# Optimization experiments

Measured on AMD Instinct MI355X. Metric: run time of the kernel, lower is better.

## Reference

```python
import jax, jax.numpy as jnp
import numpy as np

N = 100000
E = 1600000
IN_C = 64
HID = 128
EPS = 1e-5


def _glorot(key, shape):
    fan_in, fan_out = shape[1], shape[0]
    lim = float(np.sqrt(6.0 / (fan_in + fan_out)))
    return jax.random.uniform(key, shape, jnp.float32, -lim, lim)


def setup_inputs() -> dict:
    key = jax.random.key(0)
    ks = jax.random.split(key, 12)
    x = jax.random.normal(ks[0], (N, IN_C), jnp.float32)
    edge_index = jax.random.randint(ks[1], (2, E), 0, N, jnp.int64)
    return {
        "x": x,
        "edge_index": edge_index,
        # SAGEConv layer 0: lin_l (neighbor, with bias), lin_r (root, no bias)
        "Wl0": _glorot(ks[2], (HID, IN_C)), "bl0": jnp.zeros((HID,), jnp.float32),
        "Wr0": _glorot(ks[3], (HID, IN_C)),
        "g0": jnp.ones((HID,), jnp.float32), "be0": jnp.zeros((HID,), jnp.float32),
        # SAGEConv layer 1
        "Wl1": _glorot(ks[4], (HID, HID)), "bl1": jnp.zeros((HID,), jnp.float32),
        "Wr1": _glorot(ks[5], (HID, HID)),
        "g1": jnp.ones((HID,), jnp.float32), "be1": jnp.zeros((HID,), jnp.float32),
        # MLP head: hidden -> hidden//2 -> 1
        "W1": _glorot(ks[6], (HID // 2, HID)), "b1": jnp.zeros((HID // 2,), jnp.float32),
        "W2": _glorot(ks[7], (1, HID // 2)), "b2": jnp.zeros((1,), jnp.float32),
    }


def _sage_max(x, src, dst, Wl, bl, Wr):
    # gather source features along edges, scatter-max into destination nodes
    msgs = x[src]                                             # [E, d]
    agg = jax.ops.segment_max(msgs, dst, num_segments=N)      # [N, d], -inf if empty
    agg = jnp.where(jnp.isfinite(agg), agg, 0.0)              # empty neighborhoods -> 0 (PyG scatter)
    return agg @ Wl.T + bl + x @ Wr.T


def _layernorm(x, g, b):
    mu = jnp.mean(x, axis=-1, keepdims=True)
    var = jnp.var(x, axis=-1, keepdims=True)
    return (x - mu) * jax.lax.rsqrt(var + EPS) * g + b


def reference(x, edge_index, Wl0, bl0, Wr0, g0, be0, Wl1, bl1, Wr1, g1, be1, W1, b1, W2, b2):
    src, dst = edge_index[0], edge_index[1]
    h = _sage_max(x, src, dst, Wl0, bl0, Wr0)
    h = jax.nn.relu(_layernorm(h, g0, be0))
    # dropout inactive in inference mode
    h = _sage_max(h, src, dst, Wl1, bl1, Wr1)
    h = jax.nn.relu(_layernorm(h, g1, be1))
    h = jax.nn.relu(h @ W1.T + b1)
    h = h @ W2.T + b2                                         # [N, 1]
    return jax.nn.sigmoid(h)[:, 0]                            # [N]
```

## Files before the change

kernel.cpp:

```cpp
#include <hip/hip_runtime.h>
#include <math.h>


static inline int ceil_div(int a, int b) { return (a + b - 1) / b; }

typedef unsigned int uint;
typedef __attribute__((ext_vector_type(8))) short short8;
typedef __attribute__((ext_vector_type(4))) float f32x4;

#define NBSHIFT 8
#define ACHUNK 4096
#define BCAP 6144

#define QMAX 8.0f
#define QSCL (255.0f / QMAX)
#define QINV (QMAX / 255.0f)

__device__ __forceinline__ unsigned short f2bf(float f) {
  uint u = __float_as_uint(f);
  u += 0x7fffu + ((u >> 16) & 1u);
  return (unsigned short)(u >> 16);
}
__device__ __forceinline__ float bfval(unsigned short b) {
  return __uint_as_float((uint)b << 16);
}
__device__ __forceinline__ uint pack2(float lo, float hi) {
  return (uint)f2bf(lo) | ((uint)f2bf(hi) << 16);
}
__device__ __forceinline__ uint pkmaxu16(uint a, uint b) {
  uint r;
  asm("v_pk_max_u16 %0, %1, %2" : "=v"(r) : "v"(a), "v"(b));
  return r;
}
__device__ __forceinline__ uint pk_exact(uint b0, uint b1) {
  return (__float_as_uint((float)b0) >> 16) |
         (__float_as_uint((float)b1) & 0xFFFF0000u);
}


__global__ __launch_bounds__(256) void k_fprep(
    const float* __restrict__ x, uint* __restrict__ xb, uint* __restrict__ xm,
    int total, const int* __restrict__ dst, int* __restrict__ gbtot, int E,
    const float* __restrict__ Wl0, const float* __restrict__ Wr0,
    const float* __restrict__ Wl1, const float* __restrict__ Wr1,
    const float* __restrict__ W1m,
    uint4* __restrict__ wB0, uint4* __restrict__ wB1, uint4* __restrict__ wBm,
    int prepB, int bhistB) {
  __shared__ int bcnt[512];
  int bid = blockIdx.x, tid = threadIdx.x;
  if (bid < prepB) {
    int i = bid * 256 + tid;
    if (i < total) {
      float2 v = ((const float2*)x)[i];
      uint p = pack2(v.x, v.y);
      xb[i] = p;
      uint lo = p & 0xFFFFu, hi = p >> 16;
      lo = (lo & 0x8000u) ? (~lo & 0xFFFFu) : (lo | 0x8000u);
      hi = (hi & 0x8000u) ? (~hi & 0xFFFFu) : (hi | 0x8000u);
      xm[i] = lo | (hi << 16);
    }
  } else if (bid < prepB + bhistB) {
    int cb = bid - prepB;
    for (int i = tid; i < 512; i += 256) bcnt[i] = 0;
    __syncthreads();
    int c0 = cb * ACHUNK;
    int cend = min(c0 + ACHUNK, E);
    for (int e = c0 + tid; e < cend; e += 256)
      atomicAdd(&bcnt[dst[e] >> NBSHIFT], 1);
    __syncthreads();
    for (int i = tid; i < 512; i += 256) {
      int c = bcnt[i];
      if (c) atomicAdd(&gbtot[i], c);
    }
  } else {
    int i = (bid - prepB - bhistB) * 256 + tid;
    if (i < 4096) {
      int lane = i & 63, jt = (i >> 6) & 7, ks = i >> 9;
      int m = lane & 15, q = lane >> 4;
      int j = jt * 16 + m;
      int half = ks >> 2;
      int kk = (ks & 3) * 32 + q * 8;
      const float* srcr = (kk < 64) ? (Wl0 + (size_t)j * 64 + kk)
                                    : (Wr0 + (size_t)j * 64 + (kk - 64));
      float4 w0 = ((const float4*)srcr)[0];
      float4 w1 = ((const float4*)srcr)[1];
      float v[8] = {w0.x, w0.y, w0.z, w0.w, w1.x, w1.y, w1.z, w1.w};
      unsigned short b16[8];
#pragma unroll
      for (int t = 0; t < 8; t++) {
        unsigned short hi = f2bf(v[t]);
        b16[t] = half ? f2bf(v[t] - bfval(hi)) : hi;
      }
      uint4 p;
      p.x = (uint)b16[0] | ((uint)b16[1] << 16);
      p.y = (uint)b16[2] | ((uint)b16[3] << 16);
      p.z = (uint)b16[4] | ((uint)b16[5] << 16);
      p.w = (uint)b16[6] | ((uint)b16[7] << 16);
      wB0[i] = p;
    } else if (i < 8192) {
      int e = i - 4096;
      int lane = e & 63, jt = (e >> 6) & 7, ks = e >> 9;
      int m = lane & 15, q = lane >> 4;
      int j = jt * 16 + m;
      int k0 = ks * 32 + q * 8;
      const float* srcr = (k0 < 128) ? (Wl1 + (size_t)j * 128 + k0)
                                     : (Wr1 + (size_t)j * 128 + (k0 - 128));
      float sc = (k0 < 128) ? QINV : 1.0f;
      float4 w0 = ((const float4*)srcr)[0];
      float4 w1 = ((const float4*)srcr)[1];
      uint4 p;
      p.x = pack2(w0.x * sc, w0.y * sc);
      p.y = pack2(w0.z * sc, w0.w * sc);
      p.z = pack2(w1.x * sc, w1.y * sc);
      p.w = pack2(w1.z * sc, w1.w * sc);
      wB1[e] = p;
    } else if (i < 9216) {
      int e = i - 8192;
      int lane = e & 63, jt = (e >> 6) & 3, ks = e >> 8;
      int m = lane & 15, q = lane >> 4;
      int j = jt * 16 + m;
      int k0 = ks * 32 + q * 8;
      const float* srcr = W1m + (size_t)j * 128 + k0;
      float4 w0 = ((const float4*)srcr)[0];
      float4 w1 = ((const float4*)srcr)[1];
      uint4 p;
      p.x = pack2(w0.x, w0.y);
      p.y = pack2(w0.z, w0.w);
      p.z = pack2(w1.x, w1.y);
      p.w = pack2(w1.z, w1.w);
      wBm[e] = p;
    }
  }
}


__global__ __launch_bounds__(256) void k_passA(const int* __restrict__ src,
                                               const int* __restrict__ dst,
                                               const int* __restrict__ gbtot,
                                               int* __restrict__ gbcur,
                                               uint* __restrict__ bed, int E) {
  __shared__ int bcnt[512];
  __shared__ int lbase[512];
  __shared__ int bbase[512];
  __shared__ int lcur[512];
  __shared__ int sgx[512];
  __shared__ int2 sbed[ACHUNK];
  int tid = threadIdx.x;
  int c0 = blockIdx.x * ACHUNK;
  int cend = min(c0 + ACHUNK, E);
  int total = cend - c0;
  for (int i = tid; i < 512; i += 256) {
    bcnt[i] = 0;
    sgx[i] = gbtot[i];
  }
  __syncthreads();
  int og0 = sgx[tid], og1 = sgx[tid + 256];
  for (int e = c0 + tid; e < cend; e += 256)
    atomicAdd(&bcnt[dst[e] >> NBSHIFT], 1);
  __syncthreads();
  for (int i = tid; i < 512; i += 256) lbase[i] = bcnt[i];
  __syncthreads();
  for (int off = 1; off < 512; off <<= 1) {
    int i0 = tid, i1 = tid + 256;
    int v0 = (i0 >= off) ? lbase[i0 - off] : 0;
    int v1 = (i1 >= off) ? lbase[i1 - off] : 0;
    int g0 = (i0 >= off) ? sgx[i0 - off] : 0;
    int g1 = (i1 >= off) ? sgx[i1 - off] : 0;
    __syncthreads();
    lbase[i0] += v0;
    lbase[i1] += v1;
    sgx[i0] += g0;
    sgx[i1] += g1;
    __syncthreads();
  }
#pragma unroll
  for (int k = 0; k < 2; k++) {
    int i = tid + k * 256;
    int c = bcnt[i];
    int gex = sgx[i] - (k ? og1 : og0);
    bbase[i] = (c > 0) ? (gex + atomicAdd(&gbcur[i], c)) : 0;
    lcur[i] = 0;
  }
  __syncthreads();
  for (int e = c0 + tid; e < cend; e += 256) {
    int s = src[e], d = dst[e];
    int b = d >> NBSHIFT;
    int lp = atomicAdd(&lcur[b], 1);
    sbed[lbase[b] - bcnt[b] + lp] = make_int2(s, d);
  }
  __syncthreads();
  for (int j = tid; j < total; j += 256) {
    int2 pr = sbed[j];
    int b = pr.y >> NBSHIFT;
    bed[bbase[b] + (j - (lbase[b] - bcnt[b]))] =
        ((uint)pr.x << 8) | ((uint)pr.y & 255u);
  }
}


__global__ __launch_bounds__(256) void k_passB(const uint* __restrict__ bed,
                                               const int* __restrict__ gbtot,
                                               int* __restrict__ counts,
                                               int* __restrict__ rowst,
                                               int* __restrict__ csr, int N, int E) {
  __shared__ int cnt[256];
  __shared__ int scn[256];
  __shared__ int lcur[256];
  __shared__ int sgx[512];
  __shared__ int scsr[BCAP];
  int b = blockIdx.x, tid = threadIdx.x;
  sgx[tid] = gbtot[tid];
  sgx[tid + 256] = gbtot[tid + 256];
  __syncthreads();
  for (int off = 1; off < 512; off <<= 1) {
    int i0 = tid, i1 = tid + 256;
    int v0 = (i0 >= off) ? sgx[i0 - off] : 0;
    int v1 = (i1 >= off) ? sgx[i1 - off] : 0;
    __syncthreads();
    sgx[i0] += v0;
    sgx[i1] += v1;
    __syncthreads();
  }
  int n0 = b << NBSHIFT;
  int n1 = min(n0 + 256, N);
  int e1 = sgx[b];
  int e0 = e1 - gbtot[b];
  int sz = e1 - e0;
  cnt[tid] = 0;
  __syncthreads();
  for (int e = e0 + tid; e < e1; e += 256)
    atomicAdd(&cnt[bed[e] & 255u], 1);
  __syncthreads();
  scn[tid] = cnt[tid];
  __syncthreads();
  for (int off = 1; off < 256; off <<= 1) {
    int t = (tid >= off) ? scn[tid - off] : 0;
    __syncthreads();
    scn[tid] += t;
    __syncthreads();
  }
  int ex = scn[tid] - cnt[tid];
  if (n0 + tid < n1) {
    counts[n0 + tid] = cnt[tid];
    rowst[n0 + tid] = e0 + ex;
  }
  lcur[tid] = ex;
  __syncthreads();
  if (sz <= BCAP) {
    for (int e = e0 + tid; e < e1; e += 256) {
      uint pr = bed[e];
      int p = atomicAdd(&lcur[pr & 255u], 1);
      scsr[p] = (int)(pr >> 8);
    }
    __syncthreads();
    for (int j = tid; j < sz; j += 256) csr[e0 + j] = scsr[j];
  } else {
    for (int e = e0 + tid; e < e1; e += 256) {
      uint pr = bed[e];
      int p = atomicAdd(&lcur[pr & 255u], 1);
      csr[e0 + p] = (int)(pr >> 8);
    }
  }
}


__global__ __launch_bounds__(256) void k_agg0b(const uint* __restrict__ xm,
                                               const int* __restrict__ rowst,
                                               const int* __restrict__ deg,
                                               const int* __restrict__ csr,
                                               uint* __restrict__ agg, int N) {
  int lane = threadIdx.x & 63;
  int sub = lane >> 5, ll = lane & 31;
  int h = sub << 5;
  int w = (blockIdx.x * 256 + threadIdx.x) >> 6;
  int nw = (gridDim.x * 256) >> 6;
  for (int n0 = w * 2; n0 < N; n0 += nw * 2) {
    int n = n0 + sub;
    bool valid = (n < N);
    int myn = valid ? n : (N - 1);
    int rs = rowst[myn], d = deg[myn];
    int dmax = max(d, __shfl_xor(d, 32));
    int fb = (d > 0) ? csr[rs] : 0;
    uint m = 0;
    for (int base = 0; base < dmax; base += 32) {
      int cnt = min(max(d - base, 0), 32);
      int cmax = min(dmax - base, 32);
      int idx = (ll < cnt) ? csr[rs + base + ll] : fb;
      for (int j = 0; j < cmax; j += 8) {
        uint u0 = xm[(size_t)__shfl(idx, h + j + 0) * 32 + ll];
        uint u1 = xm[(size_t)__shfl(idx, h + j + 1) * 32 + ll];
        uint u2 = xm[(size_t)__shfl(idx, h + j + 2) * 32 + ll];
        uint u3 = xm[(size_t)__shfl(idx, h + j + 3) * 32 + ll];
        uint u4 = xm[(size_t)__shfl(idx, h + j + 4) * 32 + ll];
        uint u5 = xm[(size_t)__shfl(idx, h + j + 5) * 32 + ll];
        uint u6 = xm[(size_t)__shfl(idx, h + j + 6) * 32 + ll];
        uint u7 = xm[(size_t)__shfl(idx, h + j + 7) * 32 + ll];
        m = pkmaxu16(m, pkmaxu16(pkmaxu16(pkmaxu16(u0, u1), pkmaxu16(u2, u3)),
                                 pkmaxu16(pkmaxu16(u4, u5), pkmaxu16(u6, u7))));
      }
    }
    if (valid) {
      uint lo = m & 0xFFFFu, hi = m >> 16;
      lo = (lo & 0x8000u) ? (lo ^ 0x8000u) : (~lo & 0xFFFFu);
      hi = (hi & 0x8000u) ? (hi ^ 0x8000u) : (~hi & 0xFFFFu);
      agg[(size_t)n * 32 + ll] = (d > 0) ? (lo | (hi << 16)) : 0u;
    }
  }
}


__global__ __launch_bounds__(256) void k_agg1q(const uint* __restrict__ hq,
                                               const int* __restrict__ rowst,
                                               const int* __restrict__ deg,
                                               const int* __restrict__ csr,
                                               uint* __restrict__ aggq, int N) {
  int lane = threadIdx.x & 63;
  int sub = lane >> 5, ll = lane & 31;
  int h = sub << 5;
  int w = (blockIdx.x * 256 + threadIdx.x) >> 6;
  int nw = (gridDim.x * 256) >> 6;
  for (int n0 = w * 2; n0 < N; n0 += nw * 2) {
    int n = n0 + sub;
    bool valid = (n < N);
    int myn = valid ? n : (N - 1);
    int rs = rowst[myn], d = deg[myn];
    int dmax = max(d, __shfl_xor(d, 32));
    int fb = (d > 0) ? csr[rs] : 0;
    uint me = 0, mo = 0;
    for (int base = 0; base < dmax; base += 32) {
      int cnt = min(max(d - base, 0), 32);
      int cmax = min(dmax - base, 32);
      int idx = (ll < cnt) ? csr[rs + base + ll] : fb;
      for (int j = 0; j < cmax; j += 8) {
        uint v0 = hq[(size_t)__shfl(idx, h + j + 0) * 32 + ll];
        uint v1 = hq[(size_t)__shfl(idx, h + j + 1) * 32 + ll];
        uint v2 = hq[(size_t)__shfl(idx, h + j + 2) * 32 + ll];
        uint v3 = hq[(size_t)__shfl(idx, h + j + 3) * 32 + ll];
        uint v4 = hq[(size_t)__shfl(idx, h + j + 4) * 32 + ll];
        uint v5 = hq[(size_t)__shfl(idx, h + j + 5) * 32 + ll];
        uint v6 = hq[(size_t)__shfl(idx, h + j + 6) * 32 + ll];
        uint v7 = hq[(size_t)__shfl(idx, h + j + 7) * 32 + ll];
        uint e01 = pkmaxu16(v0 & 0x00FF00FFu, v1 & 0x00FF00FFu);
        uint e23 = pkmaxu16(v2 & 0x00FF00FFu, v3 & 0x00FF00FFu);
        uint e45 = pkmaxu16(v4 & 0x00FF00FFu, v5 & 0x00FF00FFu);
        uint e67 = pkmaxu16(v6 & 0x00FF00FFu, v7 & 0x00FF00FFu);
        uint o01 = pkmaxu16(v0 & 0xFF00FF00u, v1 & 0xFF00FF00u);
        uint o23 = pkmaxu16(v2 & 0xFF00FF00u, v3 & 0xFF00FF00u);
        uint o45 = pkmaxu16(v4 & 0xFF00FF00u, v5 & 0xFF00FF00u);
        uint o67 = pkmaxu16(v6 & 0xFF00FF00u, v7 & 0xFF00FF00u);
        me = pkmaxu16(me, pkmaxu16(pkmaxu16(e01, e23), pkmaxu16(e45, e67)));
        mo = pkmaxu16(mo, pkmaxu16(pkmaxu16(o01, o23), pkmaxu16(o45, o67)));
      }
    }
    if (valid) aggq[(size_t)n * 32 + ll] = (d > 0) ? (me | mo) : 0u;
  }
}


__global__ __launch_bounds__(256) void k_lin0(
    const uint* __restrict__ agg,
    const uint* __restrict__ xb,
    const uint4* __restrict__ wB,
    const float* __restrict__ bl, const float* __restrict__ g,
    const float* __restrict__ be, unsigned short* __restrict__ hout,
    unsigned char* __restrict__ hq, int N) {
  __shared__ uint4 swB[4096];
  int tid = threadIdx.x;
  for (int i = tid; i < 4096; i += 256) swB[i] = wB[i];
  __syncthreads();
  int lane = tid & 63, m = lane & 15, q = lane >> 4;
  int w = (blockIdx.x * 256 + tid) >> 6;
  int nw = (gridDim.x * 256) >> 6;
  int pairs = (N + 31) / 32;
  float blv[8], gv[8], bev[8];
#pragma unroll
  for (int jt = 0; jt < 8; jt++) {
    blv[jt] = bl[jt * 16 + m];
    gv[jt] = g[jt * 16 + m];
    bev[jt] = be[jt * 16 + m];
  }
  for (int p = w; p < pairs; p += nw) {
    int b0 = p * 32;
    short8 a[2][4];
#pragma unroll
    for (int t = 0; t < 2; t++) {
      int row = min(b0 + t * 16 + m, N - 1);
      const uint* r0 = agg + (size_t)row * 32;
      const uint* r1 = xb + (size_t)row * 32;
#pragma unroll
      for (int ks = 0; ks < 4; ks++) {
        const uint* base = (ks < 2) ? r0 : r1;
        a[t][ks] = __builtin_bit_cast(short8, *(const uint4*)(base + (ks & 1) * 16 + q * 4));
      }
    }
    f32x4 acc[2][8];
#pragma unroll
    for (int t = 0; t < 2; t++)
#pragma unroll
      for (int jt = 0; jt < 8; jt++) acc[t][jt] = {0.f, 0.f, 0.f, 0.f};
#pragma unroll
    for (int ks = 0; ks < 8; ks++) {
#pragma unroll
      for (int jt = 0; jt < 8; jt++) {
        short8 b = __builtin_bit_cast(short8, swB[(ks * 8 + jt) * 64 + lane]);
        acc[0][jt] = __builtin_amdgcn_mfma_f32_16x16x32_bf16(a[0][ks & 3], b, acc[0][jt], 0, 0, 0);
        acc[1][jt] = __builtin_amdgcn_mfma_f32_16x16x32_bf16(a[1][ks & 3], b, acc[1][jt], 0, 0, 0);
      }
    }
#pragma unroll
    for (int t = 0; t < 2; t++) {
      float s1[4] = {0.f, 0.f, 0.f, 0.f}, s2[4] = {0.f, 0.f, 0.f, 0.f};
#pragma unroll
      for (int jt = 0; jt < 8; jt++) {
        float bb = blv[jt];
#pragma unroll
        for (int r = 0; r < 4; r++) {
          float v = acc[t][jt][r] + bb;
          s1[r] += v;
          s2[r] += v * v;
        }
      }
#pragma unroll
      for (int off = 1; off < 16; off <<= 1) {
#pragma unroll
        for (int r = 0; r < 4; r++) {
          s1[r] += __shfl_xor(s1[r], off);
          s2[r] += __shfl_xor(s2[r], off);
        }
      }
      float mu[4], rstd[4];
#pragma unroll
      for (int r = 0; r < 4; r++) {
        mu[r] = s1[r] * (1.0f / 128.0f);
        float var = s2[r] * (1.0f / 128.0f) - mu[r] * mu[r];
        rstd[r] = rsqrtf(var + 1e-5f);
      }
      int nodeb = b0 + t * 16 + q * 4;
#pragma unroll
      for (int jt = 0; jt < 8; jt++) {
        float bb = blv[jt];
#pragma unroll
        for (int r = 0; r < 4; r++) {
          int node = nodeb + r;
          if (node < N) {
            float v = acc[t][jt][r] + bb;
            float o = fmaxf((v - mu[r]) * rstd[r] * gv[jt] + bev[jt], 0.0f);
            hout[(size_t)node * 128 + jt * 16 + m] = f2bf(o);
            hq[(size_t)node * 128 + jt * 16 + m] =
                (unsigned char)__float2int_rn(fminf(o * QSCL, 255.0f));
          }
        }
      }
    }
  }
}


__global__ __launch_bounds__(256) void k_lin1m(
    const uint* __restrict__ aggq,
    const uint* __restrict__ h0,
    const uint4* __restrict__ wB,
    const float* __restrict__ bl, const float* __restrict__ g,
    const float* __restrict__ be,
    const uint4* __restrict__ wBm, const float* __restrict__ b1,
    const float* __restrict__ W2, const float* __restrict__ b2,
    float* __restrict__ out, int N) {
  __shared__ uint4 swB[4096];
  __shared__ uint smlp[4][16 * 64];
  int tid = threadIdx.x;
  for (int i = tid; i < 4096; i += 256) swB[i] = wB[i];
  __syncthreads();
  int lane = tid & 63, m = lane & 15, q = lane >> 4;
  uint* sh = smlp[tid >> 6];
  unsigned short* shh = (unsigned short*)sh;
  int w = (blockIdx.x * 256 + tid) >> 6;
  int nw = (gridDim.x * 256) >> 6;
  int pairs = (N + 31) / 32;
  float blv[8], gv[8], bev[8];
#pragma unroll
  for (int jt = 0; jt < 8; jt++) {
    blv[jt] = bl[jt * 16 + m];
    gv[jt] = g[jt * 16 + m];
    bev[jt] = be[jt * 16 + m];
  }
  float b1v[4], w2v[4];
#pragma unroll
  for (int jt = 0; jt < 4; jt++) {
    b1v[jt] = b1[jt * 16 + m];
    w2v[jt] = W2[jt * 16 + m];
  }
  float b2v = b2[0];
  for (int p = w; p < pairs; p += nw) {
    int b0 = p * 32;
    short8 a[2][8];
#pragma unroll
    for (int t = 0; t < 2; t++) {
      int row = min(b0 + t * 16 + m, N - 1);
      const uint* rq = aggq + (size_t)row * 32;
      const uint* r1 = h0 + (size_t)row * 64;
#pragma unroll
      for (int ks = 0; ks < 4; ks++) {
        uint2 vv = *(const uint2*)(rq + ks * 8 + q * 2);
        uint4 pk;
        pk.x = pk_exact(vv.x & 0xFFu, (vv.x >> 8) & 0xFFu);
        pk.y = pk_exact((vv.x >> 16) & 0xFFu, vv.x >> 24);
        pk.z = pk_exact(vv.y & 0xFFu, (vv.y >> 8) & 0xFFu);
        pk.w = pk_exact((vv.y >> 16) & 0xFFu, vv.y >> 24);
        a[t][ks] = __builtin_bit_cast(short8, pk);
      }
#pragma unroll
      for (int ks = 4; ks < 8; ks++)
        a[t][ks] = __builtin_bit_cast(short8, *(const uint4*)(r1 + (ks & 3) * 16 + q * 4));
    }
    f32x4 acc[2][8];
#pragma unroll
    for (int t = 0; t < 2; t++)
#pragma unroll
      for (int jt = 0; jt < 8; jt++) acc[t][jt] = {0.f, 0.f, 0.f, 0.f};
#pragma unroll
    for (int ks = 0; ks < 8; ks++) {
#pragma unroll
      for (int jt = 0; jt < 8; jt++) {
        short8 b = __builtin_bit_cast(short8, swB[(ks * 8 + jt) * 64 + lane]);
        acc[0][jt] = __builtin_amdgcn_mfma_f32_16x16x32_bf16(a[0][ks], b, acc[0][jt], 0, 0, 0);
        acc[1][jt] = __builtin_amdgcn_mfma_f32_16x16x32_bf16(a[1][ks], b, acc[1][jt], 0, 0, 0);
      }
    }
#pragma unroll
    for (int t = 0; t < 2; t++) {
      float s1[4] = {0.f, 0.f, 0.f, 0.f}, s2[4] = {0.f, 0.f, 0.f, 0.f};
#pragma unroll
      for (int jt = 0; jt < 8; jt++) {
        float bb = blv[jt];
#pragma unroll
        for (int r = 0; r < 4; r++) {
          float v = acc[t][jt][r] + bb;
          s1[r] += v;
          s2[r] += v * v;
        }
      }
#pragma unroll
      for (int off = 1; off < 16; off <<= 1) {
#pragma unroll
        for (int r = 0; r < 4; r++) {
          s1[r] += __shfl_xor(s1[r], off);
          s2[r] += __shfl_xor(s2[r], off);
        }
      }
      float mu[4], rstd[4];
#pragma unroll
      for (int r = 0; r < 4; r++) {
        mu[r] = s1[r] * (1.0f / 128.0f);
        float var = s2[r] * (1.0f / 128.0f) - mu[r] * mu[r];
        rstd[r] = rsqrtf(var + 1e-5f);
      }
#pragma unroll
      for (int jt = 0; jt < 8; jt++) {
        float bb = blv[jt];
#pragma unroll
        for (int r = 0; r < 4; r++) {
          float v = acc[t][jt][r] + bb;
          float o = fmaxf((v - mu[r]) * rstd[r] * gv[jt] + bev[jt], 0.0f);
          int nl = q * 4 + r;
          int hidx = (nl * 128 + jt * 16 + m) ^ ((nl & 7) << 3);
          shh[hidx] = f2bf(o);
        }
      }
      asm volatile("s_waitcnt lgkmcnt(0)" ::: "memory");
      __builtin_amdgcn_sched_barrier(0);
      {
        int rsw = (m & 7) << 2;
        short8 am[4];
#pragma unroll
        for (int ks = 0; ks < 4; ks++) {
          int widx = (m * 64 + ks * 16 + q * 4) ^ rsw;
          am[ks] = __builtin_bit_cast(short8, *(const uint4*)(sh + widx));
        }
        f32x4 accm[4];
#pragma unroll
        for (int jt = 0; jt < 4; jt++) accm[jt] = {0.f, 0.f, 0.f, 0.f};
#pragma unroll
        for (int ks = 0; ks < 4; ks++) {
#pragma unroll
          for (int jt = 0; jt < 4; jt++) {
            short8 b = __builtin_bit_cast(short8, wBm[(ks * 4 + jt) * 64 + lane]);
            accm[jt] = __builtin_amdgcn_mfma_f32_16x16x32_bf16(am[ks], b, accm[jt], 0, 0, 0);
          }
        }
        float part[4] = {0.f, 0.f, 0.f, 0.f};
#pragma unroll
        for (int jt = 0; jt < 4; jt++) {
#pragma unroll
          for (int r = 0; r < 4; r++)
            part[r] += fmaxf(accm[jt][r] + b1v[jt], 0.0f) * w2v[jt];
        }
#pragma unroll
        for (int off = 1; off < 16; off <<= 1) {
#pragma unroll
          for (int r = 0; r < 4; r++) part[r] += __shfl_xor(part[r], off);
        }
        if (m == 0) {
#pragma unroll
          for (int r = 0; r < 4; r++) {
            int node = b0 + t * 16 + q * 4 + r;
            if (node < N) out[node] = 1.0f / (1.0f + expf(-(part[r] + b2v)));
          }
        }
      }
      asm volatile("s_waitcnt lgkmcnt(0)" ::: "memory");
      __builtin_amdgcn_sched_barrier(0);
    }
  }
}


extern "C" void kernel_launch(void* const* d_in, const int* in_sizes, int n_in,
                              void* d_out, int out_size, void* d_ws, size_t ws_size,
                              hipStream_t stream) {
  const float* x = (const float*)d_in[0];
  const int* ei = (const int*)d_in[1];
  const float* Wl0 = (const float*)d_in[2];
  const float* bl0 = (const float*)d_in[3];
  const float* Wr0 = (const float*)d_in[4];
  const float* g0 = (const float*)d_in[5];
  const float* be0 = (const float*)d_in[6];
  const float* Wl1 = (const float*)d_in[7];
  const float* bl1 = (const float*)d_in[8];
  const float* Wr1 = (const float*)d_in[9];
  const float* g1 = (const float*)d_in[10];
  const float* be1 = (const float*)d_in[11];
  const float* W1 = (const float*)d_in[12];
  const float* b1 = (const float*)d_in[13];
  const float* W2 = (const float*)d_in[14];
  const float* b2 = (const float*)d_in[15];
  float* out = (float*)d_out;

  const int N = in_sizes[0] / 64;
  const int E = in_sizes[1] / 2;
  const int* src = ei;
  const int* dst = ei + E;
  const int nb = ceil_div(N, 1 << NBSHIFT);

  char* ws = (char*)d_ws;
  size_t off = 0;
  auto alloc = [&](size_t bytes) -> void* {
    void* p = ws + off;
    off = (off + bytes + 255) & ~(size_t)255;
    return p;
  };
  int* counts = (int*)alloc((size_t)N * 4);
  int* rowst = (int*)alloc((size_t)N * 4);
  int* gbtot = (int*)alloc(512 * 4);
  int* gbcur = (int*)alloc(512 * 4);
  int* csr = (int*)alloc((size_t)E * 4);
  uint* regionX = (uint*)alloc((size_t)N * 64 * 4);
  uint* h0buf = (uint*)alloc((size_t)N * 64 * 4);
  uint4* wB0 = (uint4*)alloc(4096 * 16);
  uint4* wB1 = (uint4*)alloc(4096 * 16);
  uint4* wBm = (uint4*)alloc(1024 * 16);

  uint* xb = regionX;
  unsigned char* h0q = (unsigned char*)regionX;
  uint* agg0b = regionX + (size_t)N * 32;
  uint* aggq = regionX + (size_t)N * 32;
  uint* bed = h0buf;
  uint* xm = h0buf + (size_t)N * 32;

  hipMemsetAsync(gbtot, 0, 2 * 512 * 4, stream);

  int lingrid = 512;

  int prepB = ceil_div(N * 32, 256);
  int bhistB = ceil_div(E, ACHUNK);
  int wprepB = 36;
  k_fprep<<<prepB + bhistB + wprepB, 256, 0, stream>>>(
      x, xb, xm, N * 32, dst, gbtot, E, Wl0, Wr0, Wl1, Wr1, W1,
      wB0, wB1, wBm, prepB, bhistB);
  k_passA<<<ceil_div(E, ACHUNK), 256, 0, stream>>>(src, dst, gbtot, gbcur,
                                                   bed, E);
  k_passB<<<nb, 256, 0, stream>>>(bed, gbtot, counts, rowst, csr, N, E);

  k_agg0b<<<2048, 256, 0, stream>>>(xm, rowst, counts, csr, agg0b, N);
  k_lin0<<<lingrid, 256, 0, stream>>>(agg0b, xb, wB0, bl0, g0, be0,
                                      (unsigned short*)h0buf, h0q, N);
  k_agg1q<<<2048, 256, 0, stream>>>((const uint*)h0q, rowst, counts, csr,
                                    aggq, N);
  k_lin1m<<<lingrid, 256, 0, stream>>>(aggq, h0buf, wB1, bl1, g1, be1,
                                       wBm, b1, W2, b2, out, N);
}
```

Baseline: 272.4 us.

## Quantize layer-0 gather features to 8-bit and fold offset into weights/bias

Layer-0 neighbor features are stored as offset-encoded uint8 with a fixed scale instead of order-preserving bf16, halving bytes per gathered row in the max-aggregation. The scale is folded into the Wl0 weight fragments and the 128 offset is folded into a precomputed bias, so lin0 can convert bytes to bf16 exactly. The aggregation kernel now has each half-wave load two neighbors per instruction and reduces even/odd bytes with packed u16 max. It also switches lin0 to 512-thread blocks. Clamping x to roughly ±6 with about 0.05 step adds quantization error on the first layer.

```diff
diff --git a/kernel.cpp b/kernel.cpp
--- a/kernel.cpp
+++ b/kernel.cpp
@@ -15,6 +15,9 @@
 #define QMAX 8.0f
 #define QSCL (255.0f / QMAX)
 #define QINV (QMAX / 255.0f)
+
+#define X_S (12.0f / 255.0f)
+#define X_R (255.0f / 12.0f)
 
 __device__ __forceinline__ unsigned short f2bf(float f) {
   uint u = __float_as_uint(f);
@@ -36,12 +39,17 @@
   return (__float_as_uint((float)b0) >> 16) |
          (__float_as_uint((float)b1) & 0xFFFF0000u);
 }
+__device__ __forceinline__ uint q8x(float v) {
+  int b = __float2int_rn(v * X_R) + 128;
+  return (uint)min(max(b, 0), 255);
+}
 
 
 __global__ __launch_bounds__(256) void k_fprep(
-    const float* __restrict__ x, uint* __restrict__ xb, uint* __restrict__ xm,
-    int total, const int* __restrict__ dst, int* __restrict__ gbtot, int E,
+    const float* __restrict__ x, uint* __restrict__ xb, uint* __restrict__ xm8,
+    int total16, const int* __restrict__ dst, int* __restrict__ gbtot, int E,
     const float* __restrict__ Wl0, const float* __restrict__ Wr0,
+    const float* __restrict__ bl0, float* __restrict__ bl0p,
     const float* __restrict__ Wl1, const float* __restrict__ Wr1,
     const float* __restrict__ W1m,
     uint4* __restrict__ wB0, uint4* __restrict__ wB1, uint4* __restrict__ wBm,
@@ -50,14 +58,11 @@
   int bid = blockIdx.x, tid = threadIdx.x;
   if (bid < prepB) {
     int i = bid * 256 + tid;
-    if (i < total) {
-      float2 v = ((const float2*)x)[i];
-      uint p = pack2(v.x, v.y);
-      xb[i] = p;
-      uint lo = p & 0xFFFFu, hi = p >> 16;
-      lo = (lo & 0x8000u) ? (~lo & 0xFFFFu) : (lo | 0x8000u);
-      hi = (hi & 0x8000u) ? (~hi & 0xFFFFu) : (hi | 0x8000u);
-      xm[i] = lo | (hi << 16);
+    if (i < total16) {
+      float4 v = ((const float4*)x)[i];
+      xb[i * 2] = pack2(v.x, v.y);
+      xb[i * 2 + 1] = pack2(v.z, v.w);
+      xm8[i] = q8x(v.x) | (q8x(v.y) << 8) | (q8x(v.z) << 16) | (q8x(v.w) << 24);
     }
   } else if (bid < prepB + bhistB) {
     int cb = bid - prepB;
@@ -82,9 +87,11 @@
       int kk = (ks & 3) * 32 + q * 8;
       const float* srcr = (kk < 64) ? (Wl0 + (size_t)j * 64 + kk)
                                     : (Wr0 + (size_t)j * 64 + (kk - 64));
+      float sc = (kk < 64) ? X_S : 1.0f;
       float4 w0 = ((const float4*)srcr)[0];
       float4 w1 = ((const float4*)srcr)[1];
-      float v[8] = {w0.x, w0.y, w0.z, w0.w, w1.x, w1.y, w1.z, w1.w};
+      float v[8] = {w0.x * sc, w0.y * sc, w0.z * sc, w0.w * sc,
+                    w1.x * sc, w1.y * sc, w1.z * sc, w1.w * sc};
       unsigned short b16[8];
 #pragma unroll
       for (int t = 0; t < 8; t++) {
@@ -129,6 +136,12 @@
       p.z = pack2(w1.x, w1.y);
       p.w = pack2(w1.z, w1.w);
       wBm[e] = p;
+    } else if (i < 9344) {
+      int j = i - 9216;
+      float s = 0.f;
+      const float* wr = Wl0 + (size_t)j * 64;
+      for (int k = 0; k < 64; k++) s += wr[k];
+      bl0p[j] = bl0[j] - 128.0f * X_S * s;
     }
   }
 }
@@ -264,14 +277,15 @@
 }
 
 
-__global__ __launch_bounds__(256) void k_agg0b(const uint* __restrict__ xm,
+__global__ __launch_bounds__(256) void k_agg0q(const uint* __restrict__ xm8,
                                                const int* __restrict__ rowst,
                                                const int* __restrict__ deg,
                                                const int* __restrict__ csr,
-                                               uint* __restrict__ agg, int N) {
+                                               uint* __restrict__ agg8, int N) {
   int lane = threadIdx.x & 63;
   int sub = lane >> 5, ll = lane & 31;
   int h = sub << 5;
+  int wordi = ll & 15, slot = ll >> 4;
   int w = (blockIdx.x * 256 + threadIdx.x) >> 6;
   int nw = (gridDim.x * 256) >> 6;
   for (int n0 = w * 2; n0 < N; n0 += nw * 2) {
@@ -281,30 +295,36 @@
     int rs = rowst[myn], d = deg[myn];
     int dmax = max(d, __shfl_xor(d, 32));
     int fb = (d > 0) ? csr[rs] : 0;
-    uint m = 0;
+    uint me = 0, mo = 0;
     for (int base = 0; base < dmax; base += 32) {
       int cnt = min(max(d - base, 0), 32);
       int cmax = min(dmax - base, 32);
       int idx = (ll < cnt) ? csr[rs + base + ll] : fb;
-      for (int j = 0; j < cmax; j += 8) {
-        uint u0 = xm[(size_t)__shfl(idx, h + j + 0) * 32 + ll];
-        uint u1 = xm[(size_t)__shfl(idx, h + j + 1) * 32 + ll];
-        uint u2 = xm[(size_t)__shfl(idx, h + j + 2) * 32 + ll];
-        uint u3 = xm[(size_t)__shfl(idx, h + j + 3) * 32 + ll];
-        uint u4 = xm[(size_t)__shfl(idx, h + j + 4) * 32 + ll];
-        uint u5 = xm[(size_t)__shfl(idx, h + j + 5) * 32 + ll];
-        uint u6 = xm[(size_t)__shfl(idx, h + j + 6) * 32 + ll];
-        uint u7 = xm[(size_t)__shfl(idx, h + j + 7) * 32 + ll];
-        m = pkmaxu16(m, pkmaxu16(pkmaxu16(pkmaxu16(u0, u1), pkmaxu16(u2, u3)),
-                                 pkmaxu16(pkmaxu16(u4, u5), pkmaxu16(u6, u7))));
-      }
-    }
-    if (valid) {
-      uint lo = m & 0xFFFFu, hi = m >> 16;
-      lo = (lo & 0x8000u) ? (lo ^ 0x8000u) : (~lo & 0xFFFFu);
-      hi = (hi & 0x8000u) ? (hi ^ 0x8000u) : (~hi & 0xFFFFu);
-      agg[(size_t)n * 32 + ll] = (d > 0) ? (lo | (hi << 16)) : 0u;
-    }
+      for (int j = 0; j < cmax; j += 16) {
+        uint v0 = xm8[(size_t)__shfl(idx, h + j + 0 + slot) * 16 + wordi];
+        uint v1 = xm8[(size_t)__shfl(idx, h + j + 2 + slot) * 16 + wordi];
+        uint v2 = xm8[(size_t)__shfl(idx, h + j + 4 + slot) * 16 + wordi];
+        uint v3 = xm8[(size_t)__shfl(idx, h + j + 6 + slot) * 16 + wordi];
+        uint v4 = xm8[(size_t)__shfl(idx, h + j + 8 + slot) * 16 + wordi];
+        uint v5 = xm8[(size_t)__shfl(idx, h + j + 10 + slot) * 16 + wordi];
+        uint v6 = xm8[(size_t)__shfl(idx, h + j + 12 + slot) * 16 + wordi];
+        uint v7 = xm8[(size_t)__shfl(idx, h + j + 14 + slot) * 16 + wordi];
+        uint e01 = pkmaxu16(v0 & 0x00FF00FFu, v1 & 0x00FF00FFu);
+        uint e23 = pkmaxu16(v2 & 0x00FF00FFu, v3 & 0x00FF00FFu);
+        uint e45 = pkmaxu16(v4 & 0x00FF00FFu, v5 & 0x00FF00FFu);
+        uint e67 = pkmaxu16(v6 & 0x00FF00FFu, v7 & 0x00FF00FFu);
+        uint o01 = pkmaxu16(v0 & 0xFF00FF00u, v1 & 0xFF00FF00u);
+        uint o23 = pkmaxu16(v2 & 0xFF00FF00u, v3 & 0xFF00FF00u);
+        uint o45 = pkmaxu16(v4 & 0xFF00FF00u, v5 & 0xFF00FF00u);
+        uint o67 = pkmaxu16(v6 & 0xFF00FF00u, v7 & 0xFF00FF00u);
+        me = pkmaxu16(me, pkmaxu16(pkmaxu16(e01, e23), pkmaxu16(e45, e67)));
+        mo = pkmaxu16(mo, pkmaxu16(pkmaxu16(o01, o23), pkmaxu16(o45, o67)));
+      }
+    }
+    me = pkmaxu16(me, __shfl_xor(me, 16));
+    mo = pkmaxu16(mo, __shfl_xor(mo, 16));
+    if (valid && slot == 0)
+      agg8[(size_t)n * 16 + wordi] = (d > 0) ? (me | mo) : 0x80808080u;
   }
 }
 
@@ -357,20 +377,21 @@
 }
 
 
-__global__ __launch_bounds__(256) void k_lin0(
-    const uint* __restrict__ agg,
+__global__ __launch_bounds__(512) void k_lin0(
+    const uint* __restrict__ agg8,
     const uint* __restrict__ xb,
     const uint4* __restrict__ wB,
-    const float* __restrict__ bl, const float* __restrict__ g,
+    const float* __restrict__ bl,
+    const float* __restrict__ g,
     const float* __restrict__ be, unsigned short* __restrict__ hout,
     unsigned char* __restrict__ hq, int N) {
   __shared__ uint4 swB[4096];
   int tid = threadIdx.x;
-  for (int i = tid; i < 4096; i += 256) swB[i] = wB[i];
+  for (int i = tid; i < 4096; i += 512) swB[i] = wB[i];
   __syncthreads();
   int lane = tid & 63, m = lane & 15, q = lane >> 4;
-  int w = (blockIdx.x * 256 + tid) >> 6;
-  int nw = (gridDim.x * 256) >> 6;
+  int w = (blockIdx.x * 512 + tid) >> 6;
+  int nw = (gridDim.x * 512) >> 6;
   int pairs = (N + 31) / 32;
   float blv[8], gv[8], bev[8];
 #pragma unroll
@@ -385,13 +406,21 @@
 #pragma unroll
     for (int t = 0; t < 2; t++) {
       int row = min(b0 + t * 16 + m, N - 1);
-      const uint* r0 = agg + (size_t)row * 32;
+      const uint* r0 = agg8 + (size_t)row * 16;
       const uint* r1 = xb + (size_t)row * 32;
 #pragma unroll
-      for (int ks = 0; ks < 4; ks++) {
-        const uint* base = (ks < 2) ? r0 : r1;
-        a[t][ks] = __builtin_bit_cast(short8, *(const uint4*)(base + (ks & 1) * 16 + q * 4));
-      }
+      for (int ks = 0; ks < 2; ks++) {
+        uint2 vv = *(const uint2*)(r0 + ks * 8 + q * 2);
+        uint4 pk;
+        pk.x = pk_exact(vv.x & 0xFFu, (vv.x >> 8) & 0xFFu);
+        pk.y = pk_exact((vv.x >> 16) & 0xFFu, vv.x >> 24);
+        pk.z = pk_exact(vv.y & 0xFFu, (vv.y >> 8) & 0xFFu);
+        pk.w = pk_exact((vv.y >> 16) & 0xFFu, vv.y >> 24);
+        a[t][ks] = __builtin_bit_cast(short8, pk);
+      }
+#pragma unroll
+      for (int ks = 2; ks < 4; ks++)
+        a[t][ks] = __builtin_bit_cast(short8, *(const uint4*)(r1 + (ks & 1) * 16 + q * 4));
     }
     f32x4 acc[2][8];
 #pragma unroll
@@ -652,6 +681,7 @@
   int* rowst = (int*)alloc((size_t)N * 4);
   int* gbtot = (int*)alloc(512 * 4);
   int* gbcur = (int*)alloc(512 * 4);
+  float* bl0p = (float*)alloc(128 * 4);
   int* csr = (int*)alloc((size_t)E * 4);
   uint* regionX = (uint*)alloc((size_t)N * 64 * 4);
   uint* h0buf = (uint*)alloc((size_t)N * 64 * 4);
@@ -661,30 +691,28 @@
 
   uint* xb = regionX;
   unsigned char* h0q = (unsigned char*)regionX;
-  uint* agg0b = regionX + (size_t)N * 32;
+  uint* agg8 = regionX + (size_t)N * 32;
   uint* aggq = regionX + (size_t)N * 32;
   uint* bed = h0buf;
-  uint* xm = h0buf + (size_t)N * 32;
+  uint* xm8 = h0buf + (size_t)N * 32;
 
   hipMemsetAsync(gbtot, 0, 2 * 512 * 4, stream);
 
-  int lingrid = 512;
-
-  int prepB = ceil_div(N * 32, 256);
+  int prepB = ceil_div(N * 16, 256);
   int bhistB = ceil_div(E, ACHUNK);
-  int wprepB = 36;
+  int wprepB = 37;
   k_fprep<<<prepB + bhistB + wprepB, 256, 0, stream>>>(
-      x, xb, xm, N * 32, dst, gbtot, E, Wl0, Wr0, Wl1, Wr1, W1,
+      x, xb, xm8, N * 16, dst, gbtot, E, Wl0, Wr0, bl0, bl0p, Wl1, Wr1, W1,
       wB0, wB1, wBm, prepB, bhistB);
   k_passA<<<ceil_div(E, ACHUNK), 256, 0, stream>>>(src, dst, gbtot, gbcur,
                                                    bed, E);
   k_passB<<<nb, 256, 0, stream>>>(bed, gbtot, counts, rowst, csr, N, E);
 
-  k_agg0b<<<2048, 256, 0, stream>>>(xm, rowst, counts, csr, agg0b, N);
-  k_lin0<<<lingrid, 256, 0, stream>>>(agg0b, xb, wB0, bl0, g0, be0,
-                                      (unsigned short*)h0buf, h0q, N);
+  k_agg0q<<<2048, 256, 0, stream>>>(xm8, rowst, counts, csr, agg8, N);
+  k_lin0<<<256, 512, 0, stream>>>(agg8, xb, wB0, bl0p, g0, be0,
+                                  (unsigned short*)h0buf, h0q, N);
   k_agg1q<<<2048, 256, 0, stream>>>((const uint*)h0q, rowst, counts, csr,
                                     aggq, N);
-  k_lin1m<<<lingrid, 256, 0, stream>>>(aggq, h0buf, wB1, bl1, g1, be1,
-                                       wBm, b1, W2, b2, out, N);
-}
+  k_lin1m<<<512, 256, 0, stream>>>(aggq, h0buf, wB1, bl1, g1, be1,
+                                   wBm, b1, W2, b2, out, N);
+}
```

New measurement: 249.6 us. 8.4% less time.
